# Optimization experiments

Hardware: AMD Instinct MI355X
Metric: run time of the kernel (lower is better)

## Reference

```python
import math
import jax, jax.numpy as jnp
import numpy as np

NUM_BITS = 8
NUM_CHUNKS = 16
EPS = 1e-5


def quantize_ste(x, mn, mx, num_bits=NUM_BITS):
    """Uniform affine quantize with straight-through estimator (repo's UniformQuantize,
    enforce_true_zero=False). mn/mx are treated as constants (repo casts to float())."""
    mn = jax.lax.stop_gradient(mn)
    mx = jax.lax.stop_gradient(mx)
    qmax = 2.0 ** num_bits - 1.0
    scale = jnp.maximum((mx - mn) / qmax, 1e-8)
    q = jnp.round(jnp.clip((x - mn) / scale, 0.0, qmax)) * scale + mn
    return x + jax.lax.stop_gradient(q - x)


def quant_measure(x):
    """QuantMeasure in training mode: min/max = mean over batch of per-sample min/max."""
    xf = jax.lax.stop_gradient(x.reshape(x.shape[0], -1))
    mn = xf.min(axis=-1).mean()
    mx = xf.max(axis=-1).mean()
    return quantize_ste(x, mn, mx, NUM_BITS)


def qconv2d(x, w, b, stride, padding, groups):
    """QConv2d forward: quantize input (QuantMeasure), weight and bias (per-tensor min/max),
    then standard conv. Grad quantization / biprecision only affects backward numerics."""
    qx = quant_measure(x)
    qw = quantize_ste(w, w.min(), w.max(), NUM_BITS)
    out = jax.lax.conv_general_dilated(
        qx, qw, window_strides=(stride, stride),
        padding=[(padding, padding), (padding, padding)],
        feature_group_count=groups,
        dimension_numbers=('NCHW', 'OIHW', 'NCHW'))
    if b is not None:
        qb = quantize_ste(b, b.min(), b.max(), NUM_BITS)
        out = out + qb[None, :, None, None]
    return out


def range_bn(x, weight, bias):
    """RangeBN (training mode): range-based scale estimate over NUM_CHUNKS chunks."""
    x = quant_measure(x)
    B, C, H, W = x.shape
    y = jnp.transpose(x, (1, 0, 2, 3)).reshape(C, NUM_CHUNKS, -1)  # [C, chunks, BHW/chunks]
    mean_max = y.max(axis=-1).mean(axis=-1)   # [C]
    mean_min = y.min(axis=-1).mean(axis=-1)   # [C]
    mean = y.reshape(C, -1).mean(axis=-1)     # [C]
    n = y.shape[-1]
    scale_fix = (0.5 * 0.35) * (1 + (math.pi * math.log(4)) ** 0.5) / ((2 * math.log(n)) ** 0.5)
    scale = 1.0 / ((mean_max - mean_min) * scale_fix + EPS)
    scale = quantize_ste(scale, scale.min(), scale.max(), NUM_BITS)
    out = (x - mean[None, :, None, None]) * scale[None, :, None, None]
    qw = quantize_ste(weight, weight.min(), weight.max(), NUM_BITS)
    out = out * qw[None, :, None, None]
    out = out + bias[None, :, None, None]
    return out


def setup_inputs() -> dict:
    key = jax.random.key(0)
    ks = jax.random.split(key, 8)
    B, Cin, Cout, H, W, K = 32, 256, 256, 56, 56, 3
    x = jax.random.normal(ks[0], (B, Cin, H, W), dtype=jnp.float32)
    # depthwise conv: groups=Cin -> weight [Cin, 1, K, K], kaiming-ish scale
    dw_w = jax.random.normal(ks[1], (Cin, 1, K, K), dtype=jnp.float32) * (1.0 / K)
    dw_b = jax.random.normal(ks[2], (Cin,), dtype=jnp.float32) * 0.1
    bn1_w = jax.random.uniform(ks[3], (Cin,), dtype=jnp.float32)
    bn1_b = jnp.zeros((Cin,), dtype=jnp.float32)
    # pointwise conv: [Cout, Cin, 1, 1], bias=False
    pw_w = jax.random.normal(ks[4], (Cout, Cin, 1, 1), dtype=jnp.float32) * (1.0 / math.sqrt(Cin))
    bn2_w = jax.random.uniform(ks[5], (Cout,), dtype=jnp.float32)
    bn2_b = jnp.zeros((Cout,), dtype=jnp.float32)
    return {"x": x, "dw_w": dw_w, "dw_b": dw_b, "bn1_w": bn1_w, "bn1_b": bn1_b,
            "pw_w": pw_w, "bn2_w": bn2_w, "bn2_b": bn2_b}


def reference(x, dw_w, dw_b, bn1_w, bn1_b, pw_w, bn2_w, bn2_b):
    Cin = x.shape[1]
    h = qconv2d(x, dw_w, dw_b, stride=1, padding=1, groups=Cin)  # depthwise QConv2d
    h = jax.nn.relu(range_bn(h, bn1_w, bn1_b))
    h = qconv2d(h, pw_w, None, stride=1, padding=0, groups=1)    # pointwise QConv2d (no bias)
    h = jax.nn.relu(range_bn(h, bn2_w, bn2_b))
    return h
```

## Files before the change

### kernel.cpp

```cpp
#include <hip/hip_runtime.h>
#include <math.h>

#define IMG 56
#define HW 3136
#define NCH 256
#define NB 32
#define SAMPLE (NCH*HW)
#define TOT (NB*SAMPLE)
#define ASTR 132

typedef short s16x8 __attribute__((ext_vector_type(8)));
typedef float f32x4 __attribute__((ext_vector_type(4)));


__device__ __forceinline__ float qz(float x, float mn, float scale) {
    float t = (x - mn) / scale;
    t = fminf(fmaxf(t, 0.f), 255.f);
    return rintf(t) * scale + mn;
}

__device__ __forceinline__ float codef(float x, float mn, float scale) {
    return rintf(fminf(fmaxf((x - mn) / scale, 0.f), 255.f));
}

__device__ __forceinline__ unsigned bf16u(float v) {
    return (__float_as_uint(v) >> 16) & 0xFFFFu;
}

__device__ __forceinline__ unsigned enc(float f) {
    unsigned u = __float_as_uint(f);
    return (u & 0x80000000u) ? ~u : (u ^ 0x80000000u);
}
__device__ __forceinline__ float dec(unsigned u) {
    unsigned v = (u & 0x80000000u) ? (u ^ 0x80000000u) : ~u;
    return __uint_as_float(v);
}

__device__ __forceinline__ void blk_red_minmax(float& mn, float& mx) {
    __shared__ float smn[4], smx[4];
    __syncthreads();
    #pragma unroll
    for (int o = 32; o > 0; o >>= 1) {
        mn = fminf(mn, __shfl_down(mn, o));
        mx = fmaxf(mx, __shfl_down(mx, o));
    }
    int lane = threadIdx.x & 63, w = threadIdx.x >> 6;
    if (lane == 0) { smn[w] = mn; smx[w] = mx; }
    __syncthreads();
    if (threadIdx.x == 0) {
        int nw = (int)blockDim.x >> 6;
        for (int i = 1; i < nw; i++) { mn = fminf(mn, smn[i]); mx = fmaxf(mx, smx[i]); }
    }
}

__device__ __forceinline__ void blk_red_minmax_bcast(float& mn, float& mx) {
    __shared__ float bb[2];
    blk_red_minmax(mn, mx);
    if (threadIdx.x == 0) { bb[0] = mn; bb[1] = mx; }
    __syncthreads();
    mn = bb[0]; mx = bb[1];
}

__device__ __forceinline__ float blk_red_sum(float v) {
    __shared__ float ss[4];
    __syncthreads();
    #pragma unroll
    for (int o = 32; o > 0; o >>= 1) v += __shfl_down(v, o);
    int lane = threadIdx.x & 63, w = threadIdx.x >> 6;
    if (lane == 0) ss[w] = v;
    __syncthreads();
    if (threadIdx.x == 0) {
        int nw = (int)blockDim.x >> 6;
        for (int i = 1; i < nw; i++) v += ss[i];
    }
    return v;
}


__global__ void k_init(unsigned* xsl, unsigned* pwsl, unsigned* o2mn, unsigned* o2mx, float* o2sum) {
    int i = blockIdx.x * 256 + threadIdx.x;
    o2mn[i] = 0xFFFFFFFFu; o2mx[i] = 0u; o2sum[i] = 0.f;
    if (blockIdx.x == 0) {
        if (threadIdx.x < 64) xsl[threadIdx.x] = (threadIdx.x < 32) ? 0xFFFFFFFFu : 0u;
        if (threadIdx.x == 64) { pwsl[0] = 0xFFFFFFFFu; pwsl[1] = 0u; }
    }
}

__global__ __launch_bounds__(256) void k_pwmm(const float4* __restrict__ pw4, unsigned* pwsl) {
    int i = blockIdx.x * 256 + threadIdx.x;
    float4 v = pw4[i];
    float mn = fminf(fminf(v.x, v.y), fminf(v.z, v.w));
    float mx = fmaxf(fmaxf(v.x, v.y), fmaxf(v.z, v.w));
    blk_red_minmax(mn, mx);
    if (threadIdx.x == 0) { atomicMin(&pwsl[0], enc(mn)); atomicMax(&pwsl[1], enc(mx)); }
}

__global__ __launch_bounds__(256) void k_minmax_x(const float4* __restrict__ x4, unsigned* xsl) {
    int b = blockIdx.y, blk = blockIdx.x;
    const float4* p = x4 + (size_t)b * 200704 + (size_t)blk * 12544;
    float mn = INFINITY, mx = -INFINITY;
    for (int k = threadIdx.x; k < 12544; k += 256) {
        float4 v = p[k];
        mn = fminf(mn, fminf(fminf(v.x, v.y), fminf(v.z, v.w)));
        mx = fmaxf(mx, fmaxf(fmaxf(v.x, v.y), fmaxf(v.z, v.w)));
    }
    blk_red_minmax(mn, mx);
    if (threadIdx.x == 0) {
        atomicMin(&xsl[b], enc(mn));
        atomicMax(&xsl[32 + b], enc(mx));
    }
}

__global__ void k_fin1(const float* __restrict__ dww, const float* __restrict__ dwb,
                       const unsigned* __restrict__ xsl, float* sc) {
    int tid = threadIdx.x;
    float mn = INFINITY, mx = -INFINITY;
    for (int i = tid; i < 2304; i += 256) { float v = dww[i]; mn = fminf(mn, v); mx = fmaxf(mx, v); }
    blk_red_minmax(mn, mx);
    float w1min = mn, w1max = mx;
    float v = dwb[tid]; mn = v; mx = v;
    blk_red_minmax(mn, mx);
    if (tid == 0) {
        float sm = 0.f, sx = 0.f;
        for (int i = 0; i < 32; i++) { sm += dec(xsl[i]); sx += dec(xsl[32 + i]); }
        float m = sm / 32.f, X = sx / 32.f;
        sc[0] = m;      sc[1] = fmaxf((X - m) / 255.f, 1e-8f);
        sc[2] = w1min;  sc[3] = fmaxf((w1max - w1min) / 255.f, 1e-8f);
        sc[4] = mn;     sc[5] = fmaxf((mx - mn) / 255.f, 1e-8f);
    }
}

__global__ __launch_bounds__(256) void k_dwconv(const float4* __restrict__ x4, const float* __restrict__ w,
                                                const float* __restrict__ bias, float* __restrict__ h1,
                                                const float* __restrict__ sc,
                                                float* __restrict__ h1mn, float* __restrict__ h1mx,
                                                float* __restrict__ h1sm) {
    int bc = blockIdx.x, c = bc & 255;
    __shared__ float tile[58 * 68];
    int tid = threadIdx.x;
    for (int i = tid; i < 58 * 68; i += 256) tile[i] = 0.f;
    __syncthreads();
    float mnx = sc[0], scx = sc[1];
    const float4* px = x4 + (size_t)bc * 784;
    #pragma unroll
    for (int it = 0; it < 4; it++) {
        int idx = it * 256 + tid;
        if (idx < 784) {
            int i = idx / 14, j = (idx - i * 14) * 4;
            float4 v = px[idx];
            v.x = qz(v.x, mnx, scx); v.y = qz(v.y, mnx, scx);
            v.z = qz(v.z, mnx, scx); v.w = qz(v.w, mnx, scx);
            *(float4*)&tile[(i + 1) * 68 + j + 4] = v;
        }
    }
    __syncthreads();
    float qw[9];
    #pragma unroll
    for (int k = 0; k < 9; k++) qw[k] = qz(w[c * 9 + k], sc[2], sc[3]);
    float qb = qz(bias[c], sc[4], sc[5]);
    float4* po = (float4*)(h1 + (size_t)bc * HW);
    float lmn = INFINITY, lmx = -INFINITY, lsum = 0.f;
    #pragma unroll
    for (int it = 0; it < 4; it++) {
        int idx = it * 256 + tid;
        if (idx < 784) {
            int i = idx / 14, j = (idx - i * 14) * 4;
            float o0 = qb, o1 = qb, o2v = qb, o3 = qb;
            #pragma unroll
            for (int r = 0; r < 3; r++) {
                const float* row = &tile[(i + r) * 68 + j + 3];
                float a0 = row[0];
                float4 mid = *(const float4*)&row[1];
                float a5 = row[5];
                float w0 = qw[3 * r], w1 = qw[3 * r + 1], w2 = qw[3 * r + 2];
                o0  += a0    * w0 + mid.x * w1 + mid.y * w2;
                o1  += mid.x * w0 + mid.y * w1 + mid.z * w2;
                o2v += mid.y * w0 + mid.z * w1 + mid.w * w2;
                o3  += mid.z * w0 + mid.w * w1 + a5    * w2;
            }
            po[idx] = make_float4(o0, o1, o2v, o3);
            lmn = fminf(lmn, fminf(fminf(o0, o1), fminf(o2v, o3)));
            lmx = fmaxf(lmx, fmaxf(fmaxf(o0, o1), fmaxf(o2v, o3)));
            lsum += (o0 + o1) + (o2v + o3);
        }
    }
    blk_red_minmax(lmn, lmx);
    float ls = blk_red_sum(lsum);
    if (tid == 0) { h1mn[bc] = lmn; h1mx[bc] = lmx; h1sm[bc] = ls; }
}

__global__ __launch_bounds__(256) void k_stats1(const float* __restrict__ h1mn, const float* __restrict__ h1mx,
                                                const float* __restrict__ h1sm,
                                                const float* __restrict__ bn1w, const float* __restrict__ bn1b,
                                                const unsigned* __restrict__ pwsl, float* sc,
                                                float* __restrict__ P1, float* __restrict__ Q1,
                                                float* __restrict__ A2v, float* __restrict__ B2v) {
    int tid = threadIdx.x, lane = tid & 63, w = tid >> 6;
    __shared__ float bmn[32], bmx[32], sp[4], lP[256], lQ[256];
    #pragma unroll
    for (int i = 0; i < 8; i++) {
        int b = w * 8 + i;
        float4 m4 = *(const float4*)&h1mn[b * 256 + lane * 4];
        float4 x4 = *(const float4*)&h1mx[b * 256 + lane * 4];
        float mn = fminf(fminf(m4.x, m4.y), fminf(m4.z, m4.w));
        float mx = fmaxf(fmaxf(x4.x, x4.y), fmaxf(x4.z, x4.w));
        #pragma unroll
        for (int o = 32; o > 0; o >>= 1) { mn = fminf(mn, __shfl_down(mn, o)); mx = fmaxf(mx, __shfl_down(mx, o)); }
        if (lane == 0) { bmn[b] = mn; bmx[b] = mx; }
    }
    __syncthreads();
    if (tid == 0) {
        float sm = 0.f, sx = 0.f;
        for (int i = 0; i < 32; i++) { sm += bmn[i]; sx += bmx[i]; }
        float m = sm / 32.f, X = sx / 32.f;
        sp[0] = m; sp[1] = fmaxf((X - m) / 255.f, 1e-8f);
        sc[6] = sp[0]; sc[7] = sp[1];
        sc[14] = 1.f / sp[1];
        sc[15] = -sp[0] / sp[1];
        float pmn = dec(pwsl[0]), pmx = dec(pwsl[1]);
        sc[10] = pmn; sc[11] = fmaxf((pmx - pmn) / 255.f, 1e-8f);
    }
    __syncthreads();
    float mn1 = sp[0], s1 = sp[1];
    int c = tid;
    float mmax = 0.f, mmin = 0.f, sum = 0.f;
    for (int ck = 0; ck < 16; ck++) {
        float c0n = h1mn[(2 * ck) * 256 + c], c1n = h1mn[(2 * ck + 1) * 256 + c];
        float c0x = h1mx[(2 * ck) * 256 + c], c1x = h1mx[(2 * ck + 1) * 256 + c];
        mmin += qz(fminf(c0n, c1n), mn1, s1);
        mmax += qz(fmaxf(c0x, c1x), mn1, s1);
        sum  += h1sm[(2 * ck) * 256 + c] + h1sm[(2 * ck + 1) * 256 + c];
    }
    mmin *= 0.0625f; mmax *= 0.0625f;
    float mean = sum / 100352.f;
    const float scale_fix = (float)(0.175 * (1.0 + sqrt(3.14159265358979323846 * log(4.0))) / sqrt(2.0 * log(6272.0)));
    float scale = 1.f / ((mmax - mmin) * scale_fix + 1e-5f);
    float ssn = scale, ssx = scale;
    blk_red_minmax_bcast(ssn, ssx);
    float wv = bn1w[c];
    float wmn = wv, wmx = wv;
    blk_red_minmax_bcast(wmn, wmx);
    float qs = qz(scale, ssn, fmaxf((ssx - ssn) / 255.f, 1e-8f));
    float qw = qz(wv, wmn, fmaxf((wmx - wmn) / 255.f, 1e-8f));
    float a1 = qs * qw;
    float be = bn1b[c] - mean * a1;
    float p1v = s1 * a1, q1v = mn1 * a1 + be;
    P1[c] = p1v; Q1[c] = q1v; lP[c] = p1v; lQ[c] = q1v;
    __syncthreads();
    #pragma unroll
    for (int i = 0; i < 8; i++) {
        int b = w * 8 + i;
        float4 m4 = *(const float4*)&h1mn[b * 256 + lane * 4];
        float4 x4 = *(const float4*)&h1mx[b * 256 + lane * 4];
        float mn = INFINITY, mx = -INFINITY;
        #pragma unroll
        for (int j = 0; j < 4; j++) {
            int cc = lane * 4 + j;
            float kn = rintf(fminf(fmaxf(((&m4.x)[j] - mn1) / s1, 0.f), 255.f));
            float kx = rintf(fminf(fmaxf(((&x4.x)[j] - mn1) / s1, 0.f), 255.f));
            float hn = fmaxf(kn * lP[cc] + lQ[cc], 0.f);
            float hx = fmaxf(kx * lP[cc] + lQ[cc], 0.f);
            mn = fminf(mn, hn); mx = fmaxf(mx, hx);
        }
        #pragma unroll
        for (int o = 32; o > 0; o >>= 1) { mn = fminf(mn, __shfl_down(mn, o)); mx = fmaxf(mx, __shfl_down(mx, o)); }
        if (lane == 0) { bmn[b] = mn; bmx[b] = mx; }
    }
    __syncthreads();
    if (tid == 0) {
        float sm = 0.f, sx = 0.f;
        for (int i = 0; i < 32; i++) { sm += bmn[i]; sx += bmx[i]; }
        float m = sm / 32.f, X = sx / 32.f;
        sp[2] = m; sp[3] = fmaxf((X - m) / 255.f, 1e-8f);
        sc[8] = sp[2]; sc[9] = sp[3];
    }
    __syncthreads();
    A2v[c] = lP[c] / sp[3];
    B2v[c] = (lQ[c] - sp[2]) / sp[3];
}

__global__ __launch_bounds__(256) void k_qw(const float* __restrict__ pw, const float* __restrict__ sc,
                                            short* __restrict__ wcodes, float* __restrict__ Wsum) {
    int co = blockIdx.x, ci = threadIdx.x;
    float kw = codef(pw[co * 256 + ci], sc[10], sc[11]);
    wcodes[co * 256 + ci] = (short)bf16u(kw);
    float s = blk_red_sum(kw);
    if (ci == 0) Wsum[co] = s;
}

__global__ __launch_bounds__(256) void k_gemm(const float* __restrict__ h1, const short* __restrict__ wcodes,
                                              const float* __restrict__ Wsum, const float* __restrict__ sc,
                                              const float* __restrict__ A2v, const float* __restrict__ B2v,
                                              float* __restrict__ o2,
                                              unsigned* o2mn, unsigned* o2mx, float* o2sum) {
    int b = blockIdx.y, p0 = blockIdx.x * 64;
    __shared__ unsigned AsU[64 * ASTR];
    __shared__ float BpW[4][64];
    __shared__ float BpT[64];
    int tid = threadIdx.x, lane = tid & 63, w = tid >> 6;
    int col = lane & 15, quad = lane >> 4;
    float A1 = sc[14], B1 = sc[15];
    const float* colp = h1 + (size_t)b * SAMPLE + p0 + lane;
    unsigned base = lane * ASTR + 32 * w;
    float bp = 0.f;
    for (int t2 = 0; t2 < 16; t2++) {
        int d0 = 2 * t2;
        int ci = 64 * w + 2 * d0;
        float v0 = colp[(size_t)ci * HW];
        float v1 = colp[(size_t)(ci + 1) * HW];
        float v2 = colp[(size_t)(ci + 2) * HW];
        float v3 = colp[(size_t)(ci + 3) * HW];
        float k0f = rintf(fminf(fmaxf(fmaf(v0, A1, B1), 0.f), 255.f));
        float k1f = rintf(fminf(fmaxf(fmaf(v1, A1, B1), 0.f), 255.f));
        float k2f = rintf(fminf(fmaxf(fmaf(v2, A1, B1), 0.f), 255.f));
        float k3f = rintf(fminf(fmaxf(fmaf(v3, A1, B1), 0.f), 255.f));
        float c0 = rintf(fminf(fmaxf(fmaf(k0f, A2v[ci],     B2v[ci]),     0.f), 255.f));
        float c1 = rintf(fminf(fmaxf(fmaf(k1f, A2v[ci + 1], B2v[ci + 1]), 0.f), 255.f));
        float c2 = rintf(fminf(fmaxf(fmaf(k2f, A2v[ci + 2], B2v[ci + 2]), 0.f), 255.f));
        float c3 = rintf(fminf(fmaxf(fmaf(k3f, A2v[ci + 3], B2v[ci + 3]), 0.f), 255.f));
        bp += (c0 + c1) + (c2 + c3);
        uint2 pk;
        pk.x = bf16u(c0) | (bf16u(c1) << 16);
        pk.y = bf16u(c2) | (bf16u(c3) << 16);
        *(uint2*)&AsU[base + d0] = pk;
    }
    BpW[w][lane] = bp;
    __syncthreads();
    const short* wb = wcodes + (size_t)(w * 64 + col) * 256 + quad * 8;
    f32x4 acc[4][4];
    #pragma unroll
    for (int i = 0; i < 4; i++)
        #pragma unroll
        for (int j = 0; j < 4; j++) acc[i][j] = (f32x4){0.f, 0.f, 0.f, 0.f};
    s16x8 bcur[4];
    #pragma unroll
    for (int nt = 0; nt < 4; nt++) bcur[nt] = *(const s16x8*)(wb + (size_t)nt * 4096);
    for (int step = 0; step < 8; step++) {
        s16x8 af[4];
        #pragma unroll
        for (int mt = 0; mt < 4; mt++)
            af[mt] = *(const s16x8*)&AsU[(size_t)(mt * 16 + col) * ASTR + step * 16 + quad * 4];
        s16x8 bnx[4];
        if (step < 7) {
            #pragma unroll
            for (int nt = 0; nt < 4; nt++) bnx[nt] = *(const s16x8*)(wb + (size_t)nt * 4096 + (step + 1) * 32);
        }
        #pragma unroll
        for (int mt = 0; mt < 4; mt++)
            #pragma unroll
            for (int nt = 0; nt < 4; nt++)
                acc[mt][nt] = __builtin_amdgcn_mfma_f32_16x16x32_bf16(af[mt], bcur[nt], acc[mt][nt], 0, 0, 0);
        if (step < 7) {
            #pragma unroll
            for (int nt = 0; nt < 4; nt++) bcur[nt] = bnx[nt];
        }
    }
    if (tid < 64) BpT[tid] = BpW[0][tid] + BpW[1][tid] + BpW[2][tid] + BpW[3][tid];
    __syncthreads();
    float alpha = sc[11] * sc[9];
    float beta  = sc[11] * sc[8];
    float gamma = sc[10] * sc[9];
    float delta = 256.f * sc[10] * sc[8];
    float Wv[4];
    #pragma unroll
    for (int nt = 0; nt < 4; nt++) Wv[nt] = Wsum[w * 64 + nt * 16 + col];
    float snn[4], sxx[4], ssm[4];
    #pragma unroll
    for (int nt = 0; nt < 4; nt++) { snn[nt] = INFINITY; sxx[nt] = -INFINITY; ssm[nt] = 0.f; }
    float* obase = o2 + ((size_t)b * HW + p0) * 256 + w * 64 + col;
    #pragma unroll
    for (int mt = 0; mt < 4; mt++) {
        float bp4[4];
        #pragma unroll
        for (int r = 0; r < 4; r++) bp4[r] = BpT[mt * 16 + quad * 4 + r];
        #pragma unroll
        for (int nt = 0; nt < 4; nt++) {
            float wterm = beta * Wv[nt] + delta;
            #pragma unroll
            for (int r = 0; r < 4; r++) {
                float val = alpha * acc[mt][nt][r] + gamma * bp4[r] + wterm;
                obase[(size_t)(mt * 16 + quad * 4 + r) * 256 + nt * 16] = val;
                snn[nt] = fminf(snn[nt], val);
                sxx[nt] = fmaxf(sxx[nt], val);
                ssm[nt] += val;
            }
        }
    }
    #pragma unroll
    for (int nt = 0; nt < 4; nt++) {
        snn[nt] = fminf(snn[nt], __shfl_xor(snn[nt], 16));
        sxx[nt] = fmaxf(sxx[nt], __shfl_xor(sxx[nt], 16));
        ssm[nt] += __shfl_xor(ssm[nt], 16);
        snn[nt] = fminf(snn[nt], __shfl_xor(snn[nt], 32));
        sxx[nt] = fmaxf(sxx[nt], __shfl_xor(sxx[nt], 32));
        ssm[nt] += __shfl_xor(ssm[nt], 32);
    }
    if (lane < 16) {
        #pragma unroll
        for (int nt = 0; nt < 4; nt++) {
            int idx = b * 256 + w * 64 + nt * 16 + lane;
            atomicMin(&o2mn[idx], enc(snn[nt]));
            atomicMax(&o2mx[idx], enc(sxx[nt]));
            atomicAdd(&o2sum[idx], ssm[nt]);
        }
    }
}

__global__ __launch_bounds__(256) void k_stats2(const unsigned* __restrict__ o2mnU, const unsigned* __restrict__ o2mxU,
                                                const float* __restrict__ o2sm,
                                                const float* __restrict__ bn2w, const float* __restrict__ bn2b,
                                                float* sc, float* __restrict__ P2, float* __restrict__ Q2) {
    int tid = threadIdx.x, lane = tid & 63, w = tid >> 6;
    __shared__ float bmn[32], bmx[32], sp[2];
    #pragma unroll
    for (int i = 0; i < 8; i++) {
        int b = w * 8 + i;
        uint4 um = *(const uint4*)&o2mnU[b * 256 + lane * 4];
        uint4 ux = *(const uint4*)&o2mxU[b * 256 + lane * 4];
        float mn = fminf(fminf(dec(um.x), dec(um.y)), fminf(dec(um.z), dec(um.w)));
        float mx = fmaxf(fmaxf(dec(ux.x), dec(ux.y)), fmaxf(dec(ux.z), dec(ux.w)));
        #pragma unroll
        for (int o = 32; o > 0; o >>= 1) { mn = fminf(mn, __shfl_down(mn, o)); mx = fmaxf(mx, __shfl_down(mx, o)); }
        if (lane == 0) { bmn[b] = mn; bmx[b] = mx; }
    }
    __syncthreads();
    if (tid == 0) {
        float sm = 0.f, sx = 0.f;
        for (int i = 0; i < 32; i++) { sm += bmn[i]; sx += bmx[i]; }
        float m = sm / 32.f, X = sx / 32.f;
        sp[0] = m; sp[1] = fmaxf((X - m) / 255.f, 1e-8f);
        sc[12] = sp[0]; sc[13] = sp[1];
    }
    __syncthreads();
    float mno = sp[0], so = sp[1];
    int c = tid;
    float mmax = 0.f, mmin = 0.f, sum = 0.f;
    for (int ck = 0; ck < 16; ck++) {
        float c0n = dec(o2mnU[(2 * ck) * 256 + c]), c1n = dec(o2mnU[(2 * ck + 1) * 256 + c]);
        float c0x = dec(o2mxU[(2 * ck) * 256 + c]), c1x = dec(o2mxU[(2 * ck + 1) * 256 + c]);
        mmin += qz(fminf(c0n, c1n), mno, so);
        mmax += qz(fmaxf(c0x, c1x), mno, so);
        sum  += o2sm[(2 * ck) * 256 + c] + o2sm[(2 * ck + 1) * 256 + c];
    }
    mmin *= 0.0625f; mmax *= 0.0625f;
    float mean = sum / 100352.f;
    const float scale_fix = (float)(0.175 * (1.0 + sqrt(3.14159265358979323846 * log(4.0))) / sqrt(2.0 * log(6272.0)));
    float scale = 1.f / ((mmax - mmin) * scale_fix + 1e-5f);
    float ssn = scale, ssx = scale;
    blk_red_minmax_bcast(ssn, ssx);
    float wv = bn2w[c];
    float wmn = wv, wmx = wv;
    blk_red_minmax_bcast(wmn, wmx);
    float qs = qz(scale, ssn, fmaxf((ssx - ssn) / 255.f, 1e-8f));
    float qw = qz(wv, wmn, fmaxf((wmx - wmn) / 255.f, 1e-8f));
    float a2 = qs * qw;
    float be = bn2b[c] - mean * a2;
    P2[c] = so * a2; Q2[c] = mno * a2 + be;
}

__global__ __launch_bounds__(256) void k_apply(const float* __restrict__ o2, const float* __restrict__ sc,
                                               const float* __restrict__ P2, const float* __restrict__ Q2,
                                               float* __restrict__ out) {
    __shared__ float tile[64][65];
    int b = blockIdx.z, p0 = blockIdx.x * 64, co0 = blockIdx.y * 64;
    int t = threadIdx.x, rr = t >> 4, cq = t & 15;
    float mno = sc[12], so = sc[13];
    #pragma unroll
    for (int it = 0; it < 4; it++) {
        int p = rr + 16 * it;
        float4 v = *(const float4*)&o2[((size_t)b * HW + p0 + p) * 256 + co0 + cq * 4];
        *(float4*)&tile[p][cq * 4] = v;
    }
    __syncthreads();
    #pragma unroll
    for (int it = 0; it < 4; it++) {
        int col = rr + 16 * it;
        int c = co0 + col;
        float pv = P2[c], qv = Q2[c];
        float4 r;
        #pragma unroll
        for (int j = 0; j < 4; j++) {
            float val = tile[cq * 4 + j][col];
            (&r.x)[j] = fmaxf(rintf(fminf(fmaxf((val - mno) / so, 0.f), 255.f)) * pv + qv, 0.f);
        }
        *(float4*)&out[((size_t)b * 256 + c) * HW + p0 + cq * 4] = r;
    }
}


extern "C" void kernel_launch(void* const* d_in, const int* in_sizes, int n_in,
                              void* d_out, int out_size, void* d_ws, size_t ws_size,
                              hipStream_t stream) {
    (void)in_sizes; (void)n_in; (void)out_size; (void)ws_size;
    const float* x    = (const float*)d_in[0];
    const float* dww  = (const float*)d_in[1];
    const float* dwb  = (const float*)d_in[2];
    const float* bn1w = (const float*)d_in[3];
    const float* bn1b = (const float*)d_in[4];
    const float* pww  = (const float*)d_in[5];
    const float* bn2w = (const float*)d_in[6];
    const float* bn2b = (const float*)d_in[7];

    float* h1   = (float*)d_ws;
    float* o2   = h1 + TOT;
    float* after = o2 + TOT;
    short* wcodes = (short*)after;
    float* Wsum  = after + 32768;
    float* sc    = Wsum + 256;
    unsigned* xsl   = (unsigned*)(sc + 32);
    unsigned* pwsl  = xsl + 64;
    unsigned* o2mnU = pwsl + 64;
    unsigned* o2mxU = o2mnU + 8192;
    float* o2sm = (float*)(o2mxU + 8192);
    float* h1mn = o2sm + 8192;
    float* h1mx = h1mn + 8192;
    float* h1sm = h1mx + 8192;
    float* P1 = h1sm + 8192; float* Q1 = P1 + 256;
    float* P2 = Q1 + 256;    float* Q2 = P2 + 256;
    float* A2v = Q2 + 256;   float* B2v = A2v + 256;

    k_init<<<32, 256, 0, stream>>>(xsl, pwsl, o2mnU, o2mxU, o2sm);
    k_pwmm<<<64, 256, 0, stream>>>((const float4*)pww, pwsl);
    k_minmax_x<<<dim3(16, 32), 256, 0, stream>>>((const float4*)x, xsl);
    k_fin1<<<1, 256, 0, stream>>>(dww, dwb, xsl, sc);
    k_dwconv<<<NB * NCH, 256, 0, stream>>>((const float4*)x, dww, dwb, h1, sc, h1mn, h1mx, h1sm);
    k_stats1<<<1, 256, 0, stream>>>(h1mn, h1mx, h1sm, bn1w, bn1b, pwsl, sc, P1, Q1, A2v, B2v);
    k_qw<<<256, 256, 0, stream>>>(pww, sc, wcodes, Wsum);
    k_gemm<<<dim3(49, 32), 256, 0, stream>>>(h1, wcodes, Wsum, sc, A2v, B2v, o2, o2mnU, o2mxU, o2sm);
    k_stats2<<<1, 256, 0, stream>>>(o2mnU, o2mxU, o2sm, bn2w, bn2b, sc, P2, Q2);
    k_apply<<<dim3(49, 4, 32), 256, 0, stream>>>(o2, sc, P2, Q2, (float*)d_out);
}
```

Measured before the change: 385.3 us.

## Switch pointwise GEMM to int8 MFMA and merge front min/max kernels

Replaces the bf16 MFMA pointwise GEMM with an i8 16x16x64 MFMA, storing activation and weight codes as signed bytes offset by 128 and folding the offset into the epilogue constants. Merges the x and weight min/max kernels into one launch and moves weight quantization earlier. Also zeroes only the halo of the depthwise tile and adds loop unrolls. The int8 path halves LDS and weight bytes and doubles MFMA K per instruction, at the cost of exact-integer offset algebra that must stay correct.

```diff
diff --git a/kernel.cpp b/kernel.cpp
--- a/kernel.cpp
+++ b/kernel.cpp
@@ -7,10 +7,9 @@
 #define NB 32
 #define SAMPLE (NCH*HW)
 #define TOT (NB*SAMPLE)
-#define ASTR 132
-
-typedef short s16x8 __attribute__((ext_vector_type(8)));
-typedef float f32x4 __attribute__((ext_vector_type(4)));
+#define ASTR 68
+
+typedef int i32x4 __attribute__((ext_vector_type(4)));
 
 
 __device__ __forceinline__ float qz(float x, float mn, float scale) {
@@ -21,10 +20,6 @@
 
 __device__ __forceinline__ float codef(float x, float mn, float scale) {
     return rintf(fminf(fmaxf((x - mn) / scale, 0.f), 255.f));
-}
-
-__device__ __forceinline__ unsigned bf16u(float v) {
-    return (__float_as_uint(v) >> 16) & 0xFFFFu;
 }
 
 __device__ __forceinline__ unsigned enc(float f) {
@@ -86,36 +81,42 @@
     }
 }
 
-__global__ __launch_bounds__(256) void k_pwmm(const float4* __restrict__ pw4, unsigned* pwsl) {
-    int i = blockIdx.x * 256 + threadIdx.x;
-    float4 v = pw4[i];
-    float mn = fminf(fminf(v.x, v.y), fminf(v.z, v.w));
-    float mx = fmaxf(fmaxf(v.x, v.y), fmaxf(v.z, v.w));
-    blk_red_minmax(mn, mx);
-    if (threadIdx.x == 0) { atomicMin(&pwsl[0], enc(mn)); atomicMax(&pwsl[1], enc(mx)); }
-}
-
-__global__ __launch_bounds__(256) void k_minmax_x(const float4* __restrict__ x4, unsigned* xsl) {
-    int b = blockIdx.y, blk = blockIdx.x;
-    const float4* p = x4 + (size_t)b * 200704 + (size_t)blk * 12544;
-    float mn = INFINITY, mx = -INFINITY;
-    for (int k = threadIdx.x; k < 12544; k += 256) {
-        float4 v = p[k];
-        mn = fminf(mn, fminf(fminf(v.x, v.y), fminf(v.z, v.w)));
-        mx = fmaxf(mx, fmaxf(fmaxf(v.x, v.y), fmaxf(v.z, v.w)));
-    }
-    blk_red_minmax(mn, mx);
-    if (threadIdx.x == 0) {
-        atomicMin(&xsl[b], enc(mn));
-        atomicMax(&xsl[32 + b], enc(mx));
+__global__ __launch_bounds__(256) void k_front(const float4* __restrict__ x4, const float4* __restrict__ pw4,
+                                               unsigned* xsl, unsigned* pwsl) {
+    int id = blockIdx.x;
+    if (id < 512) {
+        int b = id >> 4, blk = id & 15;
+        const float4* p = x4 + (size_t)b * 200704 + (size_t)blk * 12544;
+        float mn = INFINITY, mx = -INFINITY;
+        for (int k = threadIdx.x; k < 12544; k += 256) {
+            float4 v = p[k];
+            mn = fminf(mn, fminf(fminf(v.x, v.y), fminf(v.z, v.w)));
+            mx = fmaxf(mx, fmaxf(fmaxf(v.x, v.y), fmaxf(v.z, v.w)));
+        }
+        blk_red_minmax(mn, mx);
+        if (threadIdx.x == 0) {
+            atomicMin(&xsl[b], enc(mn));
+            atomicMax(&xsl[32 + b], enc(mx));
+        }
+    } else {
+        int i = (id - 512) * 256 + threadIdx.x;
+        float4 v = pw4[i];
+        float mn = fminf(fminf(v.x, v.y), fminf(v.z, v.w));
+        float mx = fmaxf(fmaxf(v.x, v.y), fmaxf(v.z, v.w));
+        blk_red_minmax(mn, mx);
+        if (threadIdx.x == 0) { atomicMin(&pwsl[0], enc(mn)); atomicMax(&pwsl[1], enc(mx)); }
     }
 }
 
 __global__ void k_fin1(const float* __restrict__ dww, const float* __restrict__ dwb,
-                       const unsigned* __restrict__ xsl, float* sc) {
+                       const unsigned* __restrict__ xsl, const unsigned* __restrict__ pwsl, float* sc) {
     int tid = threadIdx.x;
     float mn = INFINITY, mx = -INFINITY;
-    for (int i = tid; i < 2304; i += 256) { float v = dww[i]; mn = fminf(mn, v); mx = fmaxf(mx, v); }
+    #pragma unroll
+    for (int i = 0; i < 9; i++) {
+        int idx = i * 256 + tid;
+        if (idx < 2304) { float v = dww[idx]; mn = fminf(mn, v); mx = fmaxf(mx, v); }
+    }
     blk_red_minmax(mn, mx);
     float w1min = mn, w1max = mx;
     float v = dwb[tid]; mn = v; mx = v;
@@ -127,7 +128,18 @@
         sc[0] = m;      sc[1] = fmaxf((X - m) / 255.f, 1e-8f);
         sc[2] = w1min;  sc[3] = fmaxf((w1max - w1min) / 255.f, 1e-8f);
         sc[4] = mn;     sc[5] = fmaxf((mx - mn) / 255.f, 1e-8f);
-    }
+        float pmn = dec(pwsl[0]), pmx = dec(pwsl[1]);
+        sc[10] = pmn; sc[11] = fmaxf((pmx - pmn) / 255.f, 1e-8f);
+    }
+}
+
+__global__ __launch_bounds__(256) void k_qw(const float* __restrict__ pw, const float* __restrict__ sc,
+                                            char* __restrict__ wcodes, float* __restrict__ Wsum) {
+    int co = blockIdx.x, ci = threadIdx.x;
+    float kw = codef(pw[co * 256 + ci], sc[10], sc[11]);
+    wcodes[co * 256 + ci] = (char)((int)kw - 128);
+    float s = blk_red_sum(kw);
+    if (ci == 0) Wsum[co] = s;
 }
 
 __global__ __launch_bounds__(256) void k_dwconv(const float4* __restrict__ x4, const float* __restrict__ w,
@@ -138,8 +150,14 @@
     int bc = blockIdx.x, c = bc & 255;
     __shared__ float tile[58 * 68];
     int tid = threadIdx.x;
-    for (int i = tid; i < 58 * 68; i += 256) tile[i] = 0.f;
-    __syncthreads();
+    if (tid < 228) {
+        int row, col2;
+        if (tid < 58)       { row = 0;              col2 = 3 + tid; }
+        else if (tid < 116) { row = 57;             col2 = 3 + tid - 58; }
+        else if (tid < 172) { row = 1 + tid - 116;  col2 = 3; }
+        else                { row = 1 + tid - 172;  col2 = 60; }
+        tile[row * 68 + col2] = 0.f;
+    }
     float mnx = sc[0], scx = sc[1];
     const float4* px = x4 + (size_t)bc * 784;
     #pragma unroll
@@ -192,8 +210,7 @@
 __global__ __launch_bounds__(256) void k_stats1(const float* __restrict__ h1mn, const float* __restrict__ h1mx,
                                                 const float* __restrict__ h1sm,
                                                 const float* __restrict__ bn1w, const float* __restrict__ bn1b,
-                                                const unsigned* __restrict__ pwsl, float* sc,
-                                                float* __restrict__ P1, float* __restrict__ Q1,
+                                                float* sc,
                                                 float* __restrict__ A2v, float* __restrict__ B2v) {
     int tid = threadIdx.x, lane = tid & 63, w = tid >> 6;
     __shared__ float bmn[32], bmx[32], sp[4], lP[256], lQ[256];
@@ -217,13 +234,12 @@
         sc[6] = sp[0]; sc[7] = sp[1];
         sc[14] = 1.f / sp[1];
         sc[15] = -sp[0] / sp[1];
-        float pmn = dec(pwsl[0]), pmx = dec(pwsl[1]);
-        sc[10] = pmn; sc[11] = fmaxf((pmx - pmn) / 255.f, 1e-8f);
     }
     __syncthreads();
     float mn1 = sp[0], s1 = sp[1];
     int c = tid;
     float mmax = 0.f, mmin = 0.f, sum = 0.f;
+    #pragma unroll
     for (int ck = 0; ck < 16; ck++) {
         float c0n = h1mn[(2 * ck) * 256 + c], c1n = h1mn[(2 * ck + 1) * 256 + c];
         float c0x = h1mx[(2 * ck) * 256 + c], c1x = h1mx[(2 * ck + 1) * 256 + c];
@@ -245,7 +261,7 @@
     float a1 = qs * qw;
     float be = bn1b[c] - mean * a1;
     float p1v = s1 * a1, q1v = mn1 * a1 + be;
-    P1[c] = p1v; Q1[c] = q1v; lP[c] = p1v; lQ[c] = q1v;
+    lP[c] = p1v; lQ[c] = q1v;
     __syncthreads();
     #pragma unroll
     for (int i = 0; i < 8; i++) {
@@ -279,16 +295,7 @@
     B2v[c] = (lQ[c] - sp[2]) / sp[3];
 }
 
-__global__ __launch_bounds__(256) void k_qw(const float* __restrict__ pw, const float* __restrict__ sc,
-                                            short* __restrict__ wcodes, float* __restrict__ Wsum) {
-    int co = blockIdx.x, ci = threadIdx.x;
-    float kw = codef(pw[co * 256 + ci], sc[10], sc[11]);
-    wcodes[co * 256 + ci] = (short)bf16u(kw);
-    float s = blk_red_sum(kw);
-    if (ci == 0) Wsum[co] = s;
-}
-
-__global__ __launch_bounds__(256) void k_gemm(const float* __restrict__ h1, const short* __restrict__ wcodes,
+__global__ __launch_bounds__(256) void k_gemm(const float* __restrict__ h1, const char* __restrict__ wcodes,
                                               const float* __restrict__ Wsum, const float* __restrict__ sc,
                                               const float* __restrict__ A2v, const float* __restrict__ B2v,
                                               float* __restrict__ o2,
@@ -301,11 +308,11 @@
     int col = lane & 15, quad = lane >> 4;
     float A1 = sc[14], B1 = sc[15];
     const float* colp = h1 + (size_t)b * SAMPLE + p0 + lane;
-    unsigned base = lane * ASTR + 32 * w;
+    unsigned base = lane * ASTR + 16 * w;
     float bp = 0.f;
+    #pragma unroll 4
     for (int t2 = 0; t2 < 16; t2++) {
-        int d0 = 2 * t2;
-        int ci = 64 * w + 2 * d0;
+        int ci = 64 * w + 4 * t2;
         float v0 = colp[(size_t)ci * HW];
         float v1 = colp[(size_t)(ci + 1) * HW];
         float v2 = colp[(size_t)(ci + 2) * HW];
@@ -319,38 +326,39 @@
         float c2 = rintf(fminf(fmaxf(fmaf(k2f, A2v[ci + 2], B2v[ci + 2]), 0.f), 255.f));
         float c3 = rintf(fminf(fmaxf(fmaf(k3f, A2v[ci + 3], B2v[ci + 3]), 0.f), 255.f));
         bp += (c0 + c1) + (c2 + c3);
-        uint2 pk;
-        pk.x = bf16u(c0) | (bf16u(c1) << 16);
-        pk.y = bf16u(c2) | (bf16u(c3) << 16);
-        *(uint2*)&AsU[base + d0] = pk;
+        unsigned b0 = (unsigned)(((int)c0 - 128) & 0xFF);
+        unsigned b1 = (unsigned)(((int)c1 - 128) & 0xFF);
+        unsigned b2 = (unsigned)(((int)c2 - 128) & 0xFF);
+        unsigned b3 = (unsigned)(((int)c3 - 128) & 0xFF);
+        AsU[base + t2] = b0 | (b1 << 8) | (b2 << 16) | (b3 << 24);
     }
     BpW[w][lane] = bp;
     __syncthreads();
-    const short* wb = wcodes + (size_t)(w * 64 + col) * 256 + quad * 8;
-    f32x4 acc[4][4];
+    const char* wb = wcodes + (size_t)(w * 64 + col) * 256 + quad * 16;
+    i32x4 acc[4][4];
     #pragma unroll
     for (int i = 0; i < 4; i++)
         #pragma unroll
-        for (int j = 0; j < 4; j++) acc[i][j] = (f32x4){0.f, 0.f, 0.f, 0.f};
-    s16x8 bcur[4];
-    #pragma unroll
-    for (int nt = 0; nt < 4; nt++) bcur[nt] = *(const s16x8*)(wb + (size_t)nt * 4096);
-    for (int step = 0; step < 8; step++) {
-        s16x8 af[4];
+        for (int j = 0; j < 4; j++) acc[i][j] = (i32x4){0, 0, 0, 0};
+    i32x4 bcur[4];
+    #pragma unroll
+    for (int nt = 0; nt < 4; nt++) bcur[nt] = *(const i32x4*)(wb + (size_t)nt * 4096);
+    for (int step = 0; step < 4; step++) {
+        i32x4 af[4];
         #pragma unroll
         for (int mt = 0; mt < 4; mt++)
-            af[mt] = *(const s16x8*)&AsU[(size_t)(mt * 16 + col) * ASTR + step * 16 + quad * 4];
-        s16x8 bnx[4];
-        if (step < 7) {
+            af[mt] = *(const i32x4*)&AsU[(size_t)(mt * 16 + col) * ASTR + step * 16 + quad * 4];
+        i32x4 bnx[4];
+        if (step < 3) {
             #pragma unroll
-            for (int nt = 0; nt < 4; nt++) bnx[nt] = *(const s16x8*)(wb + (size_t)nt * 4096 + (step + 1) * 32);
+            for (int nt = 0; nt < 4; nt++) bnx[nt] = *(const i32x4*)(wb + (size_t)nt * 4096 + (step + 1) * 64);
         }
         #pragma unroll
         for (int mt = 0; mt < 4; mt++)
             #pragma unroll
             for (int nt = 0; nt < 4; nt++)
-                acc[mt][nt] = __builtin_amdgcn_mfma_f32_16x16x32_bf16(af[mt], bcur[nt], acc[mt][nt], 0, 0, 0);
-        if (step < 7) {
+                acc[mt][nt] = __builtin_amdgcn_mfma_i32_16x16x64_i8(af[mt], bcur[nt], acc[mt][nt], 0, 0, 0);
+        if (step < 3) {
             #pragma unroll
             for (int nt = 0; nt < 4; nt++) bcur[nt] = bnx[nt];
         }
@@ -358,9 +366,9 @@
     if (tid < 64) BpT[tid] = BpW[0][tid] + BpW[1][tid] + BpW[2][tid] + BpW[3][tid];
     __syncthreads();
     float alpha = sc[11] * sc[9];
-    float beta  = sc[11] * sc[8];
-    float gamma = sc[10] * sc[9];
-    float delta = 256.f * sc[10] * sc[8];
+    float beta  = sc[11] * sc[8] + 128.f * alpha;
+    float gamma = sc[10] * sc[9] + 128.f * alpha;
+    float delta = 256.f * sc[10] * sc[8] - 4194304.f * alpha;
     float Wv[4];
     #pragma unroll
     for (int nt = 0; nt < 4; nt++) Wv[nt] = Wsum[w * 64 + nt * 16 + col];
@@ -378,7 +386,7 @@
             float wterm = beta * Wv[nt] + delta;
             #pragma unroll
             for (int r = 0; r < 4; r++) {
-                float val = alpha * acc[mt][nt][r] + gamma * bp4[r] + wterm;
+                float val = alpha * (float)acc[mt][nt][r] + gamma * bp4[r] + wterm;
                 obase[(size_t)(mt * 16 + quad * 4 + r) * 256 + nt * 16] = val;
                 snn[nt] = fminf(snn[nt], val);
                 sxx[nt] = fmaxf(sxx[nt], val);
@@ -435,6 +443,7 @@
     float mno = sp[0], so = sp[1];
     int c = tid;
     float mmax = 0.f, mmin = 0.f, sum = 0.f;
+    #pragma unroll
     for (int ck = 0; ck < 16; ck++) {
         float c0n = dec(o2mnU[(2 * ck) * 256 + c]), c1n = dec(o2mnU[(2 * ck + 1) * 256 + c]);
         float c0x = dec(o2mxU[(2 * ck) * 256 + c]), c1x = dec(o2mxU[(2 * ck + 1) * 256 + c]);
@@ -504,8 +513,8 @@
     float* h1   = (float*)d_ws;
     float* o2   = h1 + TOT;
     float* after = o2 + TOT;
-    short* wcodes = (short*)after;
-    float* Wsum  = after + 32768;
+    char* wcodes = (char*)after;
+    float* Wsum  = after + 16384;
     float* sc    = Wsum + 256;
     unsigned* xsl   = (unsigned*)(sc + 32);
     unsigned* pwsl  = xsl + 64;
@@ -515,17 +524,15 @@
     float* h1mn = o2sm + 8192;
     float* h1mx = h1mn + 8192;
     float* h1sm = h1mx + 8192;
-    float* P1 = h1sm + 8192; float* Q1 = P1 + 256;
-    float* P2 = Q1 + 256;    float* Q2 = P2 + 256;
+    float* P2 = h1sm + 8192; float* Q2 = P2 + 256;
     float* A2v = Q2 + 256;   float* B2v = A2v + 256;
 
     k_init<<<32, 256, 0, stream>>>(xsl, pwsl, o2mnU, o2mxU, o2sm);
-    k_pwmm<<<64, 256, 0, stream>>>((const float4*)pww, pwsl);
-    k_minmax_x<<<dim3(16, 32), 256, 0, stream>>>((const float4*)x, xsl);
-    k_fin1<<<1, 256, 0, stream>>>(dww, dwb, xsl, sc);
+    k_front<<<576, 256, 0, stream>>>((const float4*)x, (const float4*)pww, xsl, pwsl);
+    k_fin1<<<1, 256, 0, stream>>>(dww, dwb, xsl, pwsl, sc);
+    k_qw<<<256, 256, 0, stream>>>(pww, sc, wcodes, Wsum);
     k_dwconv<<<NB * NCH, 256, 0, stream>>>((const float4*)x, dww, dwb, h1, sc, h1mn, h1mx, h1sm);
-    k_stats1<<<1, 256, 0, stream>>>(h1mn, h1mx, h1sm, bn1w, bn1b, pwsl, sc, P1, Q1, A2v, B2v);
-    k_qw<<<256, 256, 0, stream>>>(pww, sc, wcodes, Wsum);
+    k_stats1<<<1, 256, 0, stream>>>(h1mn, h1mx, h1sm, bn1w, bn1b, sc, A2v, B2v);
     k_gemm<<<dim3(49, 32), 256, 0, stream>>>(h1, wcodes, Wsum, sc, A2v, B2v, o2, o2mnU, o2mxU, o2sm);
     k_stats2<<<1, 256, 0, stream>>>(o2mnU, o2mxU, o2sm, bn2w, bn2b, sc, P2, Q2);
     k_apply<<<dim3(49, 4, 32), 256, 0, stream>>>(o2, sc, P2, Q2, (float*)d_out);
```

New measurement: 358.7 us. 6.9% less time.
